# Kernel optimization log

Measured on AMD Instinct MI355X. Metric: run time of the kernel, lower is better.

The kernel has to match this reference:

```python
import jax, jax.numpy as jnp
import numpy as np
from jax import lax

DILATIONS = (1, 3, 5)
EPS = 1e-5
B, T, C, S, K = 8, 4096, 512, 64, 3


def _adain(x, s, w, b):
    # instance norm over time (axis=1), per (batch, channel), no learned affine;
    # style-conditioned affine: (1+gamma)*xn + beta
    h = s @ w + b                              # (B, 2C)
    gamma, beta = jnp.split(h, 2, axis=-1)     # (B, C) each
    mu = jnp.mean(x, axis=1, keepdims=True)
    var = jnp.var(x, axis=1, keepdims=True)
    xn = (x - mu) * lax.rsqrt(var + EPS)
    return (1.0 + gamma[:, None, :]) * xn + beta[:, None, :]


def _snake(x, alpha):
    # snake activation: x + (1/a) * sin(a*x)^2
    return x + (1.0 / alpha) * jnp.sin(alpha * x) ** 2


def _wn_conv(x, v, g, b, dilation):
    # weight-normalized dilated 1d conv; v: (K, Cin, Cout), norm over (K, Cin)
    norm = jnp.sqrt(jnp.sum(v * v, axis=(0, 1), keepdims=True))
    w = g[None, None, :] * v / norm
    y = lax.conv_general_dilated(x, w, window_strides=(1,), padding='SAME',
                                 rhs_dilation=(dilation,),
                                 dimension_numbers=('NWC', 'WIO', 'NWC'))
    return y + b


def setup_inputs() -> dict:
    key = jax.random.key(0)
    ks = jax.random.split(key, 6)
    return {
        'x': jax.random.normal(ks[0], (B, T, C), dtype=jnp.float32),
        's': jax.random.normal(ks[1], (B, S), dtype=jnp.float32),
        'fc1_w': jax.random.normal(ks[2], (3, S, 2 * C), dtype=jnp.float32) * 0.02,
        'fc1_b': jnp.zeros((3, 2 * C), dtype=jnp.float32),
        'alpha1': jnp.ones((3, 1, 1, C), dtype=jnp.float32),
        'conv1_v': jax.random.normal(ks[3], (3, K, C, C), dtype=jnp.float32),
        'conv1_g': jnp.ones((3, C), dtype=jnp.float32),
        'conv1_b': jnp.zeros((3, C), dtype=jnp.float32),
        'fc2_w': jax.random.normal(ks[4], (3, S, 2 * C), dtype=jnp.float32) * 0.02,
        'fc2_b': jnp.zeros((3, 2 * C), dtype=jnp.float32),
        'alpha2': jnp.ones((3, 1, 1, C), dtype=jnp.float32),
        'conv2_v': jax.random.normal(ks[5], (3, K, C, C), dtype=jnp.float32),
        'conv2_g': jnp.ones((3, C), dtype=jnp.float32),
        'conv2_b': jnp.zeros((3, C), dtype=jnp.float32),
    }


def reference(x, s, fc1_w, fc1_b, alpha1, conv1_v, conv1_g, conv1_b,
              fc2_w, fc2_b, alpha2, conv2_v, conv2_g, conv2_b):
    for i, d in enumerate(DILATIONS):
        xt = _adain(x, s, fc1_w[i], fc1_b[i])
        xt = _snake(xt, alpha1[i])
        xt = _wn_conv(xt, conv1_v[i], conv1_g[i], conv1_b[i], d)
        xt = _adain(xt, s, fc2_w[i], fc2_b[i])
        xt = _snake(xt, alpha2[i])
        xt = _wn_conv(xt, conv2_v[i], conv2_g[i], conv2_b[i], 1)
        x = xt + x
    return x
```

## Files before the change

### kernel.cpp

```cpp
#include <hip/hip_runtime.h>
#include <hip/hip_bf16.h>

#define B_ 8
#define T_ 4096
#define C_ 512
#define S_ 64
#define KT 3
#define EPSC 1e-5f
#define PADB 5
#define RB 4128

typedef __attribute__((ext_vector_type(8))) short bf16x8;
typedef __attribute__((ext_vector_type(4))) float f32x4;
typedef __attribute__((address_space(3))) unsigned int lds_u32_t;
typedef const __attribute__((address_space(1))) unsigned int glb_u32_t;

__device__ inline unsigned short f2bf(float x) {
    __hip_bfloat16 h = __float2bfloat16(x);
    return *reinterpret_cast<unsigned short*>(&h);
}

__global__ void norm_partial(const float* __restrict__ v1, const float* __restrict__ v2,
                             float* __restrict__ normsq) {
    int j = blockIdx.y;
    int i = j >> 1;
    const float* v = ((j & 1) ? v2 : v1) + (size_t)i * KT * C_ * C_;
    int r0 = blockIdx.x * 16;
    int tid = threadIdx.x;
    float a0 = 0.f, a1 = 0.f;
    for (int r = 0; r < 16; ++r) {
        const float* row = v + (size_t)(r0 + r) * C_;
        float x = row[tid];
        float y = row[tid + 256];
        a0 += x * x; a1 += y * y;
    }
    atomicAdd(&normsq[j * C_ + tid], a0);
    atomicAdd(&normsq[j * C_ + tid + 256], a1);
}

__global__ void wt_kernel(const float* __restrict__ v1, const float* __restrict__ v2,
                          const float* __restrict__ g1, const float* __restrict__ g2,
                          const float* __restrict__ normsq, unsigned short* __restrict__ wT) {
    __shared__ float tile[64][65];
    int jk = blockIdx.y;
    int j = jk / 3, k = jk % 3;
    int i = j >> 1;
    const float* v = ((j & 1) ? v2 : v1) + ((size_t)i * KT + k) * C_ * C_;
    const float* g = ((j & 1) ? g2 : g1) + (size_t)i * C_;
    int tci = (blockIdx.x >> 3) * 64;
    int tco = (blockIdx.x & 7) * 64;
    int tid = threadIdx.x;
    int lr = tid >> 6, lc = tid & 63;
    for (int rr = 0; rr < 16; ++rr) {
        int ci = rr * 4 + lr;
        tile[ci][lc] = v[(size_t)(tci + ci) * C_ + tco + lc];
    }
    __syncthreads();
    for (int rr = 0; rr < 16; ++rr) {
        int co_l = rr * 4 + lr;
        int co = tco + co_l;
        float w = g[co] * rsqrtf(normsq[j * C_ + co]) * tile[lc][co_l];
        wT[((size_t)j * KT + k) * C_ * C_ + (size_t)co * C_ + tci + lc] = f2bf(w);
    }
}

__global__ void zero_pads(unsigned short* __restrict__ zp) {
    int q = blockIdx.x * 256 + threadIdx.x;
    int b = q >> 11, r = q & 2047;
    int row = r >> 6;
    int col = (r & 63) * 8;
    int prow = row < PADB ? row : row + T_;
    uint4 zz = make_uint4(0u, 0u, 0u, 0u);
    *(uint4*)(zp + ((size_t)b * RB + prow) * C_ + col) = zz;
}

__global__ void stats_partial(const float* __restrict__ u, float* __restrict__ ssum,
                              float* __restrict__ ssq) {
    int c = blockIdx.y * 256 + threadIdx.x;
    int b = blockIdx.z;
    int t0 = blockIdx.x * 64;
    const float* p = u + ((size_t)b * T_ + t0) * C_ + c;
    float s1 = 0.f, s2 = 0.f;
    for (int t = 0; t < 64; ++t) {
        float x = p[(size_t)t * C_];
        s1 += x; s2 += x * x;
    }
    atomicAdd(&ssum[b * C_ + c], s1);
    atomicAdd(&ssq[b * C_ + c], s2);
}

__global__ void adain_finalize(const float* __restrict__ ssum, const float* __restrict__ ssq,
                               const float* __restrict__ s, const float* __restrict__ fcw,
                               const float* __restrict__ fcb,
                               float* __restrict__ scale, float* __restrict__ shift) {
    int idx = blockIdx.x * 256 + threadIdx.x;
    int b = idx >> 9, c = idx & (C_ - 1);
    float mu = ssum[idx] * (1.f / T_);
    float var = ssq[idx] * (1.f / T_) - mu * mu;
    var = fmaxf(var, 0.f);
    float gamma = fcb[c], beta = fcb[C_ + c];
    const float* sp = s + b * S_;
    for (int p = 0; p < S_; ++p) {
        float sv = sp[p];
        gamma += sv * fcw[p * 2 * C_ + c];
        beta  += sv * fcw[p * 2 * C_ + C_ + c];
    }
    float sc = (1.f + gamma) * rsqrtf(var + EPSC);
    scale[idx] = sc;
    shift[idx] = beta - mu * sc;
}

__global__ void act_kernel(const float* __restrict__ u, const float* __restrict__ scale,
                           const float* __restrict__ shift, const float* __restrict__ alpha,
                           unsigned short* __restrict__ zp) {
    size_t idx4 = (size_t)blockIdx.x * 256 + threadIdx.x;
    size_t e0 = idx4 * 4;
    int c = (int)(e0 & (C_ - 1));
    int b = (int)(e0 >> 21);
    const float4 xv = *(const float4*)(u + e0);
    const float4 scv = *(const float4*)(scale + b * C_ + c);
    const float4 shv = *(const float4*)(shift + b * C_ + c);
    const float4 av = *(const float4*)(alpha + c);
    float xx[4] = {xv.x, xv.y, xv.z, xv.w};
    float ss[4] = {scv.x, scv.y, scv.z, scv.w};
    float hh[4] = {shv.x, shv.y, shv.z, shv.w};
    float aa[4] = {av.x, av.y, av.z, av.w};
    ushort4 o;
    unsigned short r[4];
    #pragma unroll
    for (int q = 0; q < 4; ++q) {
        float val = xx[q] * ss[q] + hh[q];
        float sn = sinf(aa[q] * val);
        r[q] = f2bf(val + sn * sn / aa[q]);
    }
    o.x = r[0]; o.y = r[1]; o.z = r[2]; o.w = r[3];
    size_t dst = ((size_t)b * RB + PADB) * C_ + (e0 & (((size_t)1 << 21) - 1));
    *(ushort4*)(zp + dst) = o;
}

#define BM 256
#define BN 256
#define AR 272

__global__ __launch_bounds__(512, 2) void conv_kernel(
    const unsigned short* __restrict__ zp, const unsigned short* __restrict__ wTj,
    const float* __restrict__ bias, const float* __restrict__ residual,
    float* __restrict__ out, float* __restrict__ ssum, float* __restrict__ ssq, int dil) {
    __shared__ __align__(16) unsigned short As[2][AR * 64];
    __shared__ __align__(16) unsigned short Bs[2][BN * 64];
    int tid = threadIdx.x;
    int wv = tid >> 6, l = tid & 63;
    int l16 = l & 15, lg = l >> 4;
    int m0 = blockIdx.x * BM;
    int b = m0 >> 12, t0 = m0 & (T_ - 1);
    int n0 = blockIdx.y * BN;
    int wm = (wv >> 2) * 128, wn = (wv & 3) * 64;
    const unsigned short* aBase = zp + ((size_t)b * RB + t0) * C_;

    f32x4 acc[8][4];
    #pragma unroll
    for (int a = 0; a < 8; ++a)
        #pragma unroll
        for (int q = 0; q < 4; ++q) acc[a][q] = (f32x4){0.f, 0.f, 0.f, 0.f};

    auto STAGE_A = [&](int ci0, int pa) {
        #pragma unroll
        for (int it = 0; it < 4; ++it) {
            int chunk = it * 512 + tid;
            int row = chunk >> 3, c = chunk & 7;
            const unsigned short* src = aBase + (size_t)row * C_ + ci0 + ((c ^ (row & 7)) * 8);
            __builtin_amdgcn_global_load_lds((glb_u32_t*)src,
                (lds_u32_t*)&As[pa][(it * 512 + wv * 64) * 8], 16, 0, 0);
        }
        if (wv < 2) {
            int chunk = 2048 + wv * 64 + l;
            int row = chunk >> 3, c = chunk & 7;
            const unsigned short* src = aBase + (size_t)row * C_ + ci0 + ((c ^ (row & 7)) * 8);
            __builtin_amdgcn_global_load_lds((glb_u32_t*)src,
                (lds_u32_t*)&As[pa][(2048 + wv * 64) * 8], 16, 0, 0);
        }
    };
    auto STAGE_B = [&](int ci0, int k, int pb) {
        #pragma unroll
        for (int it = 0; it < 4; ++it) {
            int chunk = it * 512 + tid;
            int row = chunk >> 3, c = chunk & 7;
            const unsigned short* src = wTj + ((size_t)k * C_ + n0 + row) * C_ + ci0 + ((c ^ (row & 7)) * 8);
            __builtin_amdgcn_global_load_lds((glb_u32_t*)src,
                (lds_u32_t*)&Bs[pb][(it * 512 + wv * 64) * 8], 16, 0, 0);
        }
    };

    int pa = 0, pb = 0;
    STAGE_A(0, 0);
    STAGE_B(0, 0, 0);
    __syncthreads();

    for (int ci0 = 0; ci0 < C_; ci0 += 64) {
        #pragma unroll
        for (int k = 0; k < 3; ++k) {
            if (k < 2) {
                STAGE_B(ci0, k + 1, pb ^ 1);
            } else if (ci0 < C_ - 64) {
                STAGE_B(ci0 + 64, 0, pb ^ 1);
                STAGE_A(ci0 + 64, pa ^ 1);
            }
            int sh = (k - 1) * dil + PADB;
            __builtin_amdgcn_s_setprio(1);
            #pragma unroll
            for (int ks = 0; ks < 2; ++ks) {
                bf16x8 afr[8], bfr[4];
                #pragma unroll
                for (int nf = 0; nf < 4; ++nf) {
                    int row = wn + nf * 16 + l16;
                    bfr[nf] = *(const bf16x8*)(&Bs[pb][row * 64 + (((ks * 4 + lg) ^ (row & 7)) * 8)]);
                }
                #pragma unroll
                for (int mf = 0; mf < 8; ++mf) {
                    int row = wm + mf * 16 + l16 + sh;
                    afr[mf] = *(const bf16x8*)(&As[pa][row * 64 + (((ks * 4 + lg) ^ (row & 7)) * 8)]);
                }
                #pragma unroll
                for (int mf = 0; mf < 8; ++mf)
                    #pragma unroll
                    for (int nf = 0; nf < 4; ++nf)
                        acc[mf][nf] = __builtin_amdgcn_mfma_f32_16x16x32_bf16(
                            afr[mf], bfr[nf], acc[mf][nf], 0, 0, 0);
            }
            __builtin_amdgcn_s_setprio(0);
            __syncthreads();
            pb ^= 1;
            if (k == 2) pa ^= 1;
        }
    }

    #pragma unroll
    for (int nf = 0; nf < 4; ++nf) {
        int co = n0 + wn + nf * 16 + l16;
        float bv = bias[co];
        float s1 = 0.f, s2 = 0.f;
        #pragma unroll
        for (int mf = 0; mf < 8; ++mf) {
            #pragma unroll
            for (int r = 0; r < 4; ++r) {
                int t = t0 + wm + mf * 16 + lg * 4 + r;
                size_t idx = ((size_t)b * T_ + t) * C_ + co;
                float val = acc[mf][nf][r] + bv;
                if (residual) val += residual[idx];
                out[idx] = val;
                s1 += val; s2 += val * val;
            }
        }
        s1 += __shfl_xor(s1, 16); s1 += __shfl_xor(s1, 32);
        s2 += __shfl_xor(s2, 16); s2 += __shfl_xor(s2, 32);
        if (lg == 0) {
            atomicAdd(&ssum[b * C_ + co], s1);
            atomicAdd(&ssq[b * C_ + co], s2);
        }
    }
}

extern "C" void kernel_launch(void* const* d_in, const int* in_sizes, int n_in,
                              void* d_out, int out_size, void* d_ws, size_t ws_size,
                              hipStream_t stream) {
    const float* x       = (const float*)d_in[0];
    const float* s       = (const float*)d_in[1];
    const float* fc1_w   = (const float*)d_in[2];
    const float* fc1_b   = (const float*)d_in[3];
    const float* alpha1  = (const float*)d_in[4];
    const float* conv1_v = (const float*)d_in[5];
    const float* conv1_g = (const float*)d_in[6];
    const float* conv1_b = (const float*)d_in[7];
    const float* fc2_w   = (const float*)d_in[8];
    const float* fc2_b   = (const float*)d_in[9];
    const float* alpha2  = (const float*)d_in[10];
    const float* conv2_v = (const float*)d_in[11];
    const float* conv2_g = (const float*)d_in[12];
    const float* conv2_b = (const float*)d_in[13];
    float* outp = (float*)d_out;

    char* ws = (char*)d_ws;
    const size_t MC = (size_t)B_ * T_ * C_;
    const size_t ZSZ = (size_t)B_ * RB * C_ * 2;
    unsigned short* z  = (unsigned short*)ws;
    float* y1          = (float*)(ws + ZSZ);
    unsigned short* wT = (unsigned short*)(ws + ZSZ + MC * 4);
    float* accum       = (float*)(ws + ZSZ + MC * 4 + (size_t)6 * KT * C_ * C_ * 2);
    float* normsq = accum;
    float* stats  = accum + 6 * C_;
    float* scale  = stats + 7 * 2 * B_ * C_;
    float* shift  = scale + B_ * C_;

    hipMemsetAsync(accum, 0, (size_t)(6 * C_ + 7 * 2 * B_ * C_) * sizeof(float), stream);
    zero_pads<<<64, 256, 0, stream>>>(z);
    norm_partial<<<dim3(96, 6), 256, 0, stream>>>(conv1_v, conv2_v, normsq);
    wt_kernel<<<dim3(64, 18), 256, 0, stream>>>(conv1_v, conv2_v, conv1_g, conv2_g, normsq, wT);

    const int dils[3] = {1, 3, 5};
    const float* xin = x;
    const int BC = B_ * C_;
    stats_partial<<<dim3(64, 2, 8), 256, 0, stream>>>(x, stats, stats + BC);

    for (int i = 0; i < 3; ++i) {
        float* p_in  = stats + (size_t)(2 * i) * 2 * BC;
        float* p_mid = stats + (size_t)(2 * i + 1) * 2 * BC;
        float* p_out = stats + (size_t)(2 * i + 2) * 2 * BC;

        adain_finalize<<<16, 256, 0, stream>>>(p_in, p_in + BC, s,
                                               fc1_w + (size_t)i * S_ * 2 * C_,
                                               fc1_b + (size_t)i * 2 * C_, scale, shift);
        act_kernel<<<16384, 256, 0, stream>>>(xin, scale, shift, alpha1 + (size_t)i * C_, z);
        conv_kernel<<<dim3(128, 2), 512, 0, stream>>>(
            z, wT + (size_t)(i * 2) * KT * C_ * C_, conv1_b + (size_t)i * C_,
            nullptr, y1, p_mid, p_mid + BC, dils[i]);

        adain_finalize<<<16, 256, 0, stream>>>(p_mid, p_mid + BC, s,
                                               fc2_w + (size_t)i * S_ * 2 * C_,
                                               fc2_b + (size_t)i * 2 * C_, scale, shift);
        act_kernel<<<16384, 256, 0, stream>>>(y1, scale, shift, alpha2 + (size_t)i * C_, z);
        conv_kernel<<<dim3(128, 2), 512, 0, stream>>>(
            z, wT + (size_t)(i * 2 + 1) * KT * C_ * C_, conv2_b + (size_t)i * C_,
            xin, outp, p_out, p_out + BC, 1);
        xin = outp;
    }
}
```

Baseline: 773.8 us.

## Store intermediate conv output in bf16 and replace syncthreads with vmcnt-counted barriers

The first conv of each block now writes its output as bf16 instead of fp32, and a new 8-wide activation kernel reads it back. This halves the write and read traffic for the intermediate tensor, while the AdaIN statistics are still accumulated in fp32 before rounding. The conv main loop also swaps full __syncthreads for explicit s_waitcnt vmcnt counts plus s_barrier, and assigns each wave its own contiguous A-staging chunk. This lets outstanding async LDS loads overlap with compute. The costs are extra bf16 rounding of the intermediate and the risk of incorrect hand-counted vmcnt values.

```diff
diff --git a/kernel.cpp b/kernel.cpp
--- a/kernel.cpp
+++ b/kernel.cpp
@@ -11,13 +11,20 @@
 #define RB 4128
 
 typedef __attribute__((ext_vector_type(8))) short bf16x8;
+typedef __attribute__((ext_vector_type(8))) unsigned short u16x8;
 typedef __attribute__((ext_vector_type(4))) float f32x4;
 typedef __attribute__((address_space(3))) unsigned int lds_u32_t;
 typedef const __attribute__((address_space(1))) unsigned int glb_u32_t;
 
+#define VMWAIT(N) asm volatile("s_waitcnt vmcnt(" #N ")" ::: "memory")
+#define CFENCE    asm volatile("" ::: "memory")
+
 __device__ inline unsigned short f2bf(float x) {
     __hip_bfloat16 h = __float2bfloat16(x);
     return *reinterpret_cast<unsigned short*>(&h);
+}
+__device__ inline float bf2f(unsigned short u) {
+    return __uint_as_float((unsigned)u << 16);
 }
 
 __global__ void norm_partial(const float* __restrict__ v1, const float* __restrict__ v2,
@@ -138,6 +145,34 @@
     *(ushort4*)(zp + dst) = o;
 }
 
+__global__ void act_kernel_bf16(const unsigned short* __restrict__ u,
+                                const float* __restrict__ scale,
+                                const float* __restrict__ shift,
+                                const float* __restrict__ alpha,
+                                unsigned short* __restrict__ zp) {
+    size_t idx = (size_t)blockIdx.x * 256 + threadIdx.x;
+    size_t e0 = idx * 8;
+    int c = (int)(e0 & (C_ - 1));
+    int b = (int)(e0 >> 21);
+    u16x8 uv = *(const u16x8*)(u + e0);
+    float scv[8], shv[8], av[8];
+    *(float4*)scv = *(const float4*)(scale + b * C_ + c);
+    *(float4*)(scv + 4) = *(const float4*)(scale + b * C_ + c + 4);
+    *(float4*)shv = *(const float4*)(shift + b * C_ + c);
+    *(float4*)(shv + 4) = *(const float4*)(shift + b * C_ + c + 4);
+    *(float4*)av = *(const float4*)(alpha + c);
+    *(float4*)(av + 4) = *(const float4*)(alpha + c + 4);
+    u16x8 o;
+    #pragma unroll
+    for (int q = 0; q < 8; ++q) {
+        float val = bf2f((unsigned short)uv[q]) * scv[q] + shv[q];
+        float sn = sinf(av[q] * val);
+        o[q] = f2bf(val + sn * sn / av[q]);
+    }
+    size_t dst = ((size_t)b * RB + PADB) * C_ + (e0 & (((size_t)1 << 21) - 1));
+    *(u16x8*)(zp + dst) = o;
+}
+
 #define BM 256
 #define BN 256
 #define AR 272
@@ -145,7 +180,8 @@
 __global__ __launch_bounds__(512, 2) void conv_kernel(
     const unsigned short* __restrict__ zp, const unsigned short* __restrict__ wTj,
     const float* __restrict__ bias, const float* __restrict__ residual,
-    float* __restrict__ out, float* __restrict__ ssum, float* __restrict__ ssq, int dil) {
+    void* __restrict__ outv, int out_bf16,
+    float* __restrict__ ssum, float* __restrict__ ssq, int dil) {
     __shared__ __align__(16) unsigned short As[2][AR * 64];
     __shared__ __align__(16) unsigned short Bs[2][BN * 64];
     int tid = threadIdx.x;
@@ -164,20 +200,22 @@
         for (int q = 0; q < 4; ++q) acc[a][q] = (f32x4){0.f, 0.f, 0.f, 0.f};
 
     auto STAGE_A = [&](int ci0, int pa) {
+        int cbase = wv * 272;
         #pragma unroll
         for (int it = 0; it < 4; ++it) {
-            int chunk = it * 512 + tid;
-            int row = chunk >> 3, c = chunk & 7;
+            int ch = cbase + it * 64 + l;
+            int row = ch >> 3, c = ch & 7;
             const unsigned short* src = aBase + (size_t)row * C_ + ci0 + ((c ^ (row & 7)) * 8);
             __builtin_amdgcn_global_load_lds((glb_u32_t*)src,
-                (lds_u32_t*)&As[pa][(it * 512 + wv * 64) * 8], 16, 0, 0);
-        }
-        if (wv < 2) {
-            int chunk = 2048 + wv * 64 + l;
-            int row = chunk >> 3, c = chunk & 7;
+                (lds_u32_t*)&As[pa][(cbase + it * 64) * 8], 16, 0, 0);
+        }
+        {
+            int ch = cbase + 256 + (l & 15);
+            int row = ch >> 3, c = ch & 7;
             const unsigned short* src = aBase + (size_t)row * C_ + ci0 + ((c ^ (row & 7)) * 8);
-            __builtin_amdgcn_global_load_lds((glb_u32_t*)src,
-                (lds_u32_t*)&As[pa][(2048 + wv * 64) * 8], 16, 0, 0);
+            if (l < 16)
+                __builtin_amdgcn_global_load_lds((glb_u32_t*)src,
+                    (lds_u32_t*)&As[pa][(cbase + 256) * 8], 16, 0, 0);
         }
     };
     auto STAGE_B = [&](int ci0, int k, int pb) {
@@ -191,20 +229,25 @@
         }
     };
 
-    int pa = 0, pb = 0;
     STAGE_A(0, 0);
     STAGE_B(0, 0, 0);
-    __syncthreads();
+    int pa = 0, pb = 0;
 
     for (int ci0 = 0; ci0 < C_; ci0 += 64) {
         #pragma unroll
         for (int k = 0; k < 3; ++k) {
             if (k < 2) {
                 STAGE_B(ci0, k + 1, pb ^ 1);
+                VMWAIT(4);
             } else if (ci0 < C_ - 64) {
+                STAGE_A(ci0 + 64, pa ^ 1);
                 STAGE_B(ci0 + 64, 0, pb ^ 1);
-                STAGE_A(ci0 + 64, pa ^ 1);
+                VMWAIT(9);
+            } else {
+                VMWAIT(0);
             }
+            __builtin_amdgcn_s_barrier();
+            CFENCE;
             int sh = (k - 1) * dil + PADB;
             __builtin_amdgcn_s_setprio(1);
             #pragma unroll
@@ -228,7 +271,8 @@
                             afr[mf], bfr[nf], acc[mf][nf], 0, 0, 0);
             }
             __builtin_amdgcn_s_setprio(0);
-            __syncthreads();
+            CFENCE;
+            __builtin_amdgcn_s_barrier();
             pb ^= 1;
             if (k == 2) pa ^= 1;
         }
@@ -247,7 +291,8 @@
                 size_t idx = ((size_t)b * T_ + t) * C_ + co;
                 float val = acc[mf][nf][r] + bv;
                 if (residual) val += residual[idx];
-                out[idx] = val;
+                if (out_bf16) ((unsigned short*)outv)[idx] = f2bf(val);
+                else          ((float*)outv)[idx] = val;
                 s1 += val; s2 += val * val;
             }
         }
@@ -282,10 +327,10 @@
     char* ws = (char*)d_ws;
     const size_t MC = (size_t)B_ * T_ * C_;
     const size_t ZSZ = (size_t)B_ * RB * C_ * 2;
-    unsigned short* z  = (unsigned short*)ws;
-    float* y1          = (float*)(ws + ZSZ);
-    unsigned short* wT = (unsigned short*)(ws + ZSZ + MC * 4);
-    float* accum       = (float*)(ws + ZSZ + MC * 4 + (size_t)6 * KT * C_ * C_ * 2);
+    unsigned short* z   = (unsigned short*)ws;
+    unsigned short* y1b = (unsigned short*)(ws + ZSZ);
+    unsigned short* wT  = (unsigned short*)(ws + ZSZ + MC * 4);
+    float* accum        = (float*)(ws + ZSZ + MC * 4 + (size_t)6 * KT * C_ * C_ * 2);
     float* normsq = accum;
     float* stats  = accum + 6 * C_;
     float* scale  = stats + 7 * 2 * B_ * C_;
@@ -312,15 +357,15 @@
         act_kernel<<<16384, 256, 0, stream>>>(xin, scale, shift, alpha1 + (size_t)i * C_, z);
         conv_kernel<<<dim3(128, 2), 512, 0, stream>>>(
             z, wT + (size_t)(i * 2) * KT * C_ * C_, conv1_b + (size_t)i * C_,
-            nullptr, y1, p_mid, p_mid + BC, dils[i]);
+            nullptr, y1b, 1, p_mid, p_mid + BC, dils[i]);
 
         adain_finalize<<<16, 256, 0, stream>>>(p_mid, p_mid + BC, s,
                                                fc2_w + (size_t)i * S_ * 2 * C_,
                                                fc2_b + (size_t)i * 2 * C_, scale, shift);
-        act_kernel<<<16384, 256, 0, stream>>>(y1, scale, shift, alpha2 + (size_t)i * C_, z);
+        act_kernel_bf16<<<8192, 256, 0, stream>>>(y1b, scale, shift, alpha2 + (size_t)i * C_, z);
         conv_kernel<<<dim3(128, 2), 512, 0, stream>>>(
             z, wT + (size_t)(i * 2 + 1) * KT * C_ * C_, conv2_b + (size_t)i * C_,
-            xin, outp, p_out, p_out + BC, 1);
+            xin, outp, 0, p_out, p_out + BC, 1);
         xin = outp;
     }
 }
```

After: 916.3 us. +18.4%, slower.
